# Kernel tuning notes

Hardware: AMD Instinct MI355X
Metric: run time of the kernel (lower is better)

Reference implementation:

```python
import jax, jax.numpy as jnp
import numpy as np

D_MODEL = 1024
N_HEAD = 16
D_K = D_MODEL // N_HEAD


def setup_inputs() -> dict:
    key = jax.random.key(0)
    ks = jax.random.split(key, 11)
    B, S, D = 2, 2048, D_MODEL
    scale = 1.0 / np.sqrt(D)
    inp = {
        "q": jax.random.normal(ks[0], (B, S, D), jnp.float32),
        "k": jax.random.normal(ks[1], (B, S, D), jnp.float32),
        "v": jax.random.normal(ks[2], (B, S, D), jnp.float32),
        "w_q": jax.random.normal(ks[3], (D, D), jnp.float32) * scale,
        "b_q": jnp.zeros((D,), jnp.float32),
        "w_k": jax.random.normal(ks[4], (D, D), jnp.float32) * scale,
        "b_k": jnp.zeros((D,), jnp.float32),
        "w_v": jax.random.normal(ks[5], (D, D), jnp.float32) * scale,
        "b_v": jnp.zeros((D,), jnp.float32),
        "w_o": jax.random.normal(ks[6], (D, D), jnp.float32) * scale,
        "b_o": jnp.zeros((D,), jnp.float32),
    }
    return inp


def _split_heads(x):
    # torch: chunk(n_head, dim=-1) then cat(dim=0) -> [H*B, S, d_k]
    B, S, D = x.shape
    x = x.reshape(B, S, N_HEAD, D_K)            # contiguous last-dim chunks
    return x.transpose(2, 0, 1, 3).reshape(N_HEAD * B, S, D_K)


def _merge_heads(x, B):
    # torch: chunk(n_head, dim=0) then cat(dim=-1) -> [B, S, D]
    HB, S, dk = x.shape
    x = x.reshape(N_HEAD, B, S, dk).transpose(1, 2, 0, 3)
    return x.reshape(B, S, N_HEAD * dk)


def reference(q, k, v, w_q, b_q, w_k, b_k, w_v, b_v, w_o, b_o):
    B = q.shape[0]
    qh = _split_heads(q @ w_q + b_q)            # [H*B, S, d_k]
    kh = _split_heads(k @ w_k + b_k)
    vh = _split_heads(v @ w_v + b_v)
    # scaled dot-product attention (naive, materializes scores)
    scores = jnp.einsum('bqd,bkd->bqk', qh, kh) / jnp.sqrt(jnp.float32(D_K))
    attn = jax.nn.softmax(scores, axis=-1)
    out = jnp.einsum('bqk,bkd->bqd', attn, vh)  # [H*B, S, d_k]
    out = _merge_heads(out, B)                  # [B, S, D]
    return out @ w_o + b_o
```

## Files before the change

kernel.cpp:

```cpp
#include <hip/hip_runtime.h>
#include <hip/hip_bf16.h>
#include <stdint.h>

#define DEVINL __device__ __forceinline__

typedef __attribute__((ext_vector_type(8))) short bf16x8;
typedef __attribute__((ext_vector_type(4))) short short4v;
typedef __attribute__((ext_vector_type(8))) unsigned short ushort8;
typedef __attribute__((ext_vector_type(4))) float f32x4;
typedef __attribute__((ext_vector_type(16))) float f32x16;

DEVINL unsigned short f2bf(float x) {
  union { float f; uint32_t u; } v; v.f = x;
  uint32_t u = v.u;
  u += 0x7fffu + ((u >> 16) & 1u);
  return (unsigned short)(u >> 16);
}

DEVINL uint32_t pack_bf16x2(float lo, float hi) {
  __hip_bfloat162 bb = __float22bfloat162_rn(make_float2(lo, hi));
  uint32_t r;
  __builtin_memcpy(&r, &bb, 4);
  return r;
}

DEVINL void gload_lds16(const void* g, void* l) {
  __builtin_amdgcn_global_load_lds((const __attribute__((address_space(1))) void*)g,
                                   (__attribute__((address_space(3))) void*)l, 16, 0, 0);
}

__global__ void cvt3_f32_bf16(const float* __restrict__ in0, unsigned short* __restrict__ out0,
                              const float* __restrict__ in1, unsigned short* __restrict__ out1,
                              const float* __restrict__ in2, unsigned short* __restrict__ out2,
                              int nper) {
  int nblk = gridDim.x / 3;
  int which = blockIdx.x / nblk;
  int i = ((blockIdx.x % nblk) * blockDim.x + threadIdx.x) * 8;
  if (i >= nper) return;
  const float* in = which == 0 ? in0 : which == 1 ? in1 : in2;
  unsigned short* out = which == 0 ? out0 : which == 1 ? out1 : out2;
  float4 a = *(const float4*)(in + i);
  float4 b = *(const float4*)(in + i + 4);
  ushort8 r;
  r[0] = f2bf(a.x); r[1] = f2bf(a.y); r[2] = f2bf(a.z); r[3] = f2bf(a.w);
  r[4] = f2bf(b.x); r[5] = f2bf(b.y); r[6] = f2bf(b.z); r[7] = f2bf(b.w);
  *(ushort8*)(out + i) = r;
}

__global__ __launch_bounds__(256) void transpose_w4(
    const float* __restrict__ w0, unsigned short* __restrict__ o0,
    const float* __restrict__ w1, unsigned short* __restrict__ o1,
    const float* __restrict__ w2, unsigned short* __restrict__ o2,
    const float* __restrict__ w3, unsigned short* __restrict__ o3) {
  __shared__ float tile[64][65];
  int z = blockIdx.z;
  const float* w = z == 0 ? w0 : z == 1 ? w1 : z == 2 ? w2 : w3;
  unsigned short* wt = z == 0 ? o0 : z == 1 ? o1 : z == 2 ? o2 : o3;
  int k0 = blockIdx.y * 64, n0 = blockIdx.x * 64;
  int t = threadIdx.x;
  for (int i = 0; i < 4; ++i) {
    int r = (t >> 4) + i * 16;
    int c = (t & 15) * 4;
    float4 v = *(const float4*)(w + (size_t)(k0 + r) * 1024 + n0 + c);
    tile[r][c] = v.x; tile[r][c + 1] = v.y; tile[r][c + 2] = v.z; tile[r][c + 3] = v.w;
  }
  __syncthreads();
  for (int i = 0; i < 4; ++i) {
    int rn = (t >> 4) + i * 16;
    int ck = (t & 15) * 4;
    short4v o;
    o[0] = (short)f2bf(tile[ck + 0][rn]);
    o[1] = (short)f2bf(tile[ck + 1][rn]);
    o[2] = (short)f2bf(tile[ck + 2][rn]);
    o[3] = (short)f2bf(tile[ck + 3][rn]);
    *(short4v*)(wt + (size_t)(n0 + rn) * 1024 + k0 + ck) = o;
  }
}

__global__ __launch_bounds__(256) void gemm_bt(
    const unsigned short* __restrict__ A,
    const unsigned short* __restrict__ Bt,
    const float* __restrict__ bias,
    void* __restrict__ out, float scale, int mode) {
  constexpr int K = 1024;
  __shared__ unsigned short Alds[2 * 128 * 32];
  __shared__ unsigned short Blds[2 * 64 * 32];
  int tile_m = blockIdx.x * 128;
  int tile_n = blockIdx.y * 64;
  int t = threadIdx.x, lane = t & 63, wid = t >> 6;
  int wm = wid >> 1, wn = wid & 1;
  int fr = lane & 15, fq = lane >> 4;
  f32x4 acc[4][2] = {};

  int ga0 = wid * 64 + lane, ga1 = ga0 + 256;
  int gb0 = wid * 64 + lane;
  int ra0 = ga0 >> 2, ca0 = ((ga0 & 3) ^ ((ra0 >> 1) & 3)) * 8;
  int ra1 = ga1 >> 2, ca1 = ((ga1 & 3) ^ ((ra1 >> 1) & 3)) * 8;
  int rb0 = gb0 >> 2, cb0 = ((gb0 & 3) ^ ((rb0 >> 1) & 3)) * 8;
  const unsigned short* Abase = A  + (size_t)tile_m * K;
  const unsigned short* Bbase = Bt + (size_t)tile_n * K;

  int aoff[4], boff[2];
#pragma unroll
  for (int i = 0; i < 4; ++i) {
    int r = wm * 64 + i * 16 + fr;
    aoff[i] = (r * 4 + (fq ^ ((r >> 1) & 3))) * 8;
  }
#pragma unroll
  for (int j = 0; j < 2; ++j) {
    int r = wn * 32 + j * 16 + fr;
    boff[j] = (r * 4 + (fq ^ ((r >> 1) & 3))) * 8;
  }

  auto stage = [&](int nb, int k0) {
    gload_lds16(Abase + (size_t)ra0 * K + k0 + ca0, Alds + nb * 4096 + ga0 * 8);
    gload_lds16(Abase + (size_t)ra1 * K + k0 + ca1, Alds + nb * 4096 + ga1 * 8);
    gload_lds16(Bbase + (size_t)rb0 * K + k0 + cb0, Blds + nb * 2048 + gb0 * 8);
  };
  auto compute = [&](int nb) {
    bf16x8 af[4], bfb[2];
#pragma unroll
    for (int i = 0; i < 4; ++i) af[i] = *(const bf16x8*)(Alds + nb * 4096 + aoff[i]);
#pragma unroll
    for (int j = 0; j < 2; ++j) bfb[j] = *(const bf16x8*)(Blds + nb * 2048 + boff[j]);
#pragma unroll
    for (int i = 0; i < 4; ++i)
#pragma unroll
      for (int j = 0; j < 2; ++j)
        acc[i][j] = __builtin_amdgcn_mfma_f32_16x16x32_bf16(af[i], bfb[j], acc[i][j], 0, 0, 0);
  };

  stage(0, 0);
  __syncthreads();
  for (int it = 0; it < 16; ++it) {
    int k1 = (2 * it + 1) * 32, k2 = (2 * it + 2) * 32;
    stage(1, k1);
    compute(0);
    __syncthreads();
    if (k2 < K) stage(0, k2);
    compute(1);
    __syncthreads();
  }

#pragma unroll
  for (int i = 0; i < 4; ++i) {
#pragma unroll
    for (int j = 0; j < 2; ++j) {
      int n = tile_n + wn * 32 + j * 16 + fr;
      float bv = bias[n];
      int m0 = tile_m + wm * 64 + i * 16 + fq * 4;
      if (mode == 0) {
        size_t base = (size_t)((n >> 6) * 2 + (m0 >> 11)) * (2048 * 64) + (n & 63);
#pragma unroll
        for (int r = 0; r < 4; ++r)
          ((unsigned short*)out)[base + (size_t)((m0 + r) & 2047) * 64] =
              f2bf((acc[i][j][r] + bv) * scale);
      } else if (mode == 2) {
        size_t base = (size_t)((n >> 6) * 2 + (m0 >> 11)) * (64 * 2048)
                    + (size_t)(n & 63) * 2048 + (m0 & 2047);
        short4v o;
#pragma unroll
        for (int r = 0; r < 4; ++r) o[r] = (short)f2bf(acc[i][j][r] + bv);
        *(short4v*)((unsigned short*)out + base) = o;
      } else {
#pragma unroll
        for (int r = 0; r < 4; ++r)
          ((float*)out)[(size_t)(m0 + r) * 1024 + n] = acc[i][j][r] + bv;
      }
    }
  }
}

__global__ __launch_bounds__(256) void attn_fwd(
    const unsigned short* __restrict__ Qh,
    const unsigned short* __restrict__ Kh,
    const unsigned short* __restrict__ Vtg,
    unsigned short* __restrict__ O) {
  constexpr int S = 2048, DK = 64;
  __shared__ unsigned short Klds[2 * 64 * 64];
  __shared__ unsigned short Vlds[2 * 64 * 64];
  __shared__ unsigned short Plds[4 * 32 * 72];

  int wg = blockIdx.x;
  int swz = (wg & 7) * 64 + (wg >> 3);
  int hb = swz >> 4;
  int qt = swz & 15;
  int t = threadIdx.x, lane = t & 63, wid = t >> 6;
  int lq = lane & 31, hi = lane >> 5;
  int q0 = qt * 128;

  const unsigned short* Qb = Qh  + (size_t)hb * S * DK;
  const unsigned short* Kb = Kh  + (size_t)hb * S * DK;
  const unsigned short* Vb = Vtg + (size_t)hb * DK * S;

  bf16x8 qf[4];
#pragma unroll
  for (int kk = 0; kk < 4; ++kk)
    qf[kk] = *(const bf16x8*)(Qb + (size_t)(q0 + wid * 32 + lq) * DK + kk * 16 + hi * 8);

  int g0 = wid * 128 + lane, g1 = g0 + 64;
  int sr0 = g0 >> 3, sc0 = ((g0 & 7) ^ (sr0 & 7)) * 8;
  int sr1 = g1 >> 3, sc1 = ((g1 & 7) ^ (sr1 & 7)) * 8;

  int koff[2][4], voff[2][4];
#pragma unroll
  for (int h2 = 0; h2 < 2; ++h2) {
    int row = 32 * h2 + lq;
#pragma unroll
    for (int kk = 0; kk < 4; ++kk)
      koff[h2][kk] = (row * 8 + ((2 * kk + hi) ^ (row & 7))) * 8;
  }
#pragma unroll
  for (int jt = 0; jt < 2; ++jt) {
    int row = 32 * jt + lq;
#pragma unroll
    for (int ks = 0; ks < 4; ++ks)
      voff[jt][ks] = (row * 8 + ((2 * ks + hi) ^ (row & 7))) * 8;
  }

  unsigned short* Pw = Plds + wid * (32 * 72) + lq * 72;

  auto stage = [&](int nb, int kt) {
    const unsigned short* Ksrc = Kb + (size_t)kt * 64 * DK;
    const unsigned short* Vsrc = Vb + (size_t)kt * 64;
    gload_lds16(Ksrc + sr0 * 64 + sc0, Klds + nb * 4096 + g0 * 8);
    gload_lds16(Ksrc + sr1 * 64 + sc1, Klds + nb * 4096 + g1 * 8);
    gload_lds16(Vsrc + (size_t)sr0 * S + sc0, Vlds + nb * 4096 + g0 * 8);
    gload_lds16(Vsrc + (size_t)sr1 * S + sc1, Vlds + nb * 4096 + g1 * 8);
  };

  float m = -INFINITY, l = 0.f;
  f32x16 oacc[2] = {};

  auto tilestep = [&](int nb) {
    const unsigned short* Kc = Klds + nb * 4096;
    const unsigned short* Vc = Vlds + nb * 4096;

    f32x16 sacc[2] = {};
#pragma unroll
    for (int kk = 0; kk < 4; ++kk) {
      bf16x8 k0 = *(const bf16x8*)(Kc + koff[0][kk]);
      sacc[0] = __builtin_amdgcn_mfma_f32_32x32x16_bf16(k0, qf[kk], sacc[0], 0, 0, 0);
      bf16x8 k1 = *(const bf16x8*)(Kc + koff[1][kk]);
      sacc[1] = __builtin_amdgcn_mfma_f32_32x32x16_bf16(k1, qf[kk], sacc[1], 0, 0, 0);
    }

    float pmax = fmaxf(sacc[0][0], sacc[0][1]);
#pragma unroll
    for (int r = 2; r < 16; r += 2) pmax = fmaxf(pmax, fmaxf(sacc[0][r], sacc[0][r + 1]));
#pragma unroll
    for (int r = 0; r < 16; r += 2) pmax = fmaxf(pmax, fmaxf(sacc[1][r], sacc[1][r + 1]));
    pmax = fmaxf(pmax, __shfl_xor(pmax, 32, 64));

    float mn = fmaxf(m, pmax);
    float cf = __expf(m - mn);
    m = mn;
    l *= cf;
#pragma unroll
    for (int jt = 0; jt < 2; ++jt)
#pragma unroll
      for (int r = 0; r < 16; ++r) oacc[jt][r] *= cf;

    float ps0 = 0.f, ps1 = 0.f;
#pragma unroll
    for (int r = 0; r < 16; ++r) {
      float p0 = __expf(sacc[0][r] - m);
      float p1 = __expf(sacc[1][r] - m);
      sacc[0][r] = p0; sacc[1][r] = p1;
      ps0 += p0; ps1 += p1;
    }
    float psum = ps0 + ps1;
    psum += __shfl_xor(psum, 32, 64);
    l += psum;

#pragma unroll
    for (int h2 = 0; h2 < 2; ++h2)
#pragma unroll
      for (int rp = 0; rp < 8; ++rp) {
        uint32_t w = pack_bf16x2(sacc[h2][2 * rp], sacc[h2][2 * rp + 1]);
        int key = 32 * h2 + 8 * (rp >> 1) + 4 * hi + 2 * (rp & 1);
        *(uint32_t*)(Pw + key) = w;
      }
    bf16x8 pfrag[4];
#pragma unroll
    for (int ks = 0; ks < 4; ++ks)
      pfrag[ks] = *(const bf16x8*)(Pw + 16 * ks + 8 * hi);

#pragma unroll
    for (int jt = 0; jt < 2; ++jt)
#pragma unroll
      for (int ks = 0; ks < 4; ++ks) {
        bf16x8 vf = *(const bf16x8*)(Vc + voff[jt][ks]);
        oacc[jt] = __builtin_amdgcn_mfma_f32_32x32x16_bf16(vf, pfrag[ks], oacc[jt], 0, 0, 0);
      }
  };

  stage(0, 0);
  __syncthreads();
  for (int it = 0; it < 16; ++it) {
    int t1 = 2 * it + 1, t2 = 2 * it + 2;
    stage(1, t1);
    tilestep(0);
    __syncthreads();
    if (t2 < 32) stage(0, t2);
    tilestep(1);
    __syncthreads();
  }

  int h = hb >> 1, b = hb & 1;
  int q = q0 + wid * 32 + lq;
  float linv = 1.0f / l;
  unsigned short* orow = O + (size_t)(b * 2048 + q) * 1024 + h * 64;
#pragma unroll
  for (int jt = 0; jt < 2; ++jt)
#pragma unroll
    for (int g = 0; g < 4; ++g) {
      short4v o;
#pragma unroll
      for (int r = 0; r < 4; ++r) o[r] = (short)f2bf(oacc[jt][4 * g + r] * linv);
      *(short4v*)(orow + jt * 32 + 8 * g + 4 * hi) = o;
    }
}

extern "C" void kernel_launch(void* const* d_in, const int* in_sizes, int n_in,
                              void* d_out, int out_size, void* d_ws, size_t ws_size,
                              hipStream_t stream) {
  const float* q   = (const float*)d_in[0];
  const float* k   = (const float*)d_in[1];
  const float* v   = (const float*)d_in[2];
  const float* w_q = (const float*)d_in[3];
  const float* b_q = (const float*)d_in[4];
  const float* w_k = (const float*)d_in[5];
  const float* b_k = (const float*)d_in[6];
  const float* w_v = (const float*)d_in[7];
  const float* b_v = (const float*)d_in[8];
  const float* w_o = (const float*)d_in[9];
  const float* b_o = (const float*)d_in[10];

  char* ws = (char*)d_ws;
  unsigned short* Xq  = (unsigned short*)(ws + 0);
  unsigned short* Xk  = (unsigned short*)(ws + 8388608);
  unsigned short* Xv  = (unsigned short*)(ws + 16777216);
  unsigned short* Wtq = (unsigned short*)(ws + 25165824);
  unsigned short* Wtk = (unsigned short*)(ws + 27262976);
  unsigned short* Wtv = (unsigned short*)(ws + 29360128);
  unsigned short* Wto = (unsigned short*)(ws + 31457280);
  unsigned short* Qh  = (unsigned short*)(ws + 33554432);
  unsigned short* Kh  = (unsigned short*)(ws + 41943040);
  unsigned short* Vt  = (unsigned short*)(ws + 50331648);
  unsigned short* Obuf = Xq;

  const int NACT = 4096 * 1024;
  cvt3_f32_bf16<<<3 * (NACT / 8 / 256), 256, 0, stream>>>(q, Xq, k, Xk, v, Xv, NACT);

  dim3 tg(16, 16, 4);
  transpose_w4<<<tg, 256, 0, stream>>>(w_q, Wtq, w_k, Wtk, w_v, Wtv, w_o, Wto);

  dim3 gg(32, 16);
  gemm_bt<<<gg, 256, 0, stream>>>(Xq, Wtq, b_q, Qh, 0.125f, 0);
  gemm_bt<<<gg, 256, 0, stream>>>(Xk, Wtk, b_k, Kh, 1.0f, 0);
  gemm_bt<<<gg, 256, 0, stream>>>(Xv, Wtv, b_v, Vt, 1.0f, 2);

  attn_fwd<<<512, 256, 0, stream>>>(Qh, Kh, Vt, Obuf);

  gemm_bt<<<gg, 256, 0, stream>>>(Obuf, Wto, b_o, d_out, 1.0f, 1);
}
```

Measured before the change: 169.3 us.

## Fuse QKV projections into one launch and use exp2 softmax with lazy rescale

Merges the three Q/K/V projection GEMMs into a single launch with a z-dimension that selects the operands, so the three run as one larger grid instead of three serial launches. It folds log2(e) into the Q scale so the softmax can use the hardware exp2 directly. It skips the running-max rescale of the output accumulator unless some lane's block max exceeds the stored max by more than 8, and splits the row-sum into four partial accumulators to shorten dependency chains. The lazy rescale lets exponentials reach up to 2^8 before renormalisation, which relies on fp32 headroom and bf16 packing of P staying accurate.

```diff
diff --git a/kernel.cpp b/kernel.cpp
--- a/kernel.cpp
+++ b/kernel.cpp
@@ -28,6 +28,8 @@
   __builtin_amdgcn_global_load_lds((const __attribute__((address_space(1))) void*)g,
                                    (__attribute__((address_space(3))) void*)l, 16, 0, 0);
 }
+
+#define E2(x) __builtin_amdgcn_exp2f(x)
 
 __global__ void cvt3_f32_bf16(const float* __restrict__ in0, unsigned short* __restrict__ out0,
                               const float* __restrict__ in1, unsigned short* __restrict__ out1,
@@ -77,16 +79,16 @@
   }
 }
 
-__global__ __launch_bounds__(256) void gemm_bt(
-    const unsigned short* __restrict__ A,
-    const unsigned short* __restrict__ Bt,
-    const float* __restrict__ bias,
-    void* __restrict__ out, float scale, int mode) {
+DEVINL void gemm_body(const unsigned short* __restrict__ A,
+                      const unsigned short* __restrict__ Bt,
+                      const float* __restrict__ bias,
+                      void* __restrict__ out, float scale, int mode,
+                      int bx, int by) {
   constexpr int K = 1024;
   __shared__ unsigned short Alds[2 * 128 * 32];
   __shared__ unsigned short Blds[2 * 64 * 32];
-  int tile_m = blockIdx.x * 128;
-  int tile_n = blockIdx.y * 64;
+  int tile_m = bx * 128;
+  int tile_n = by * 64;
   int t = threadIdx.x, lane = t & 63, wid = t >> 6;
   int wm = wid >> 1, wn = wid & 1;
   int fr = lane & 15, fq = lane >> 4;
@@ -171,6 +173,31 @@
   }
 }
 
+__global__ __launch_bounds__(256) void gemm_qkv(
+    const unsigned short* __restrict__ Xq, const unsigned short* __restrict__ Xk,
+    const unsigned short* __restrict__ Xv,
+    const unsigned short* __restrict__ Wtq, const unsigned short* __restrict__ Wtk,
+    const unsigned short* __restrict__ Wtv,
+    const float* __restrict__ bq, const float* __restrict__ bk,
+    const float* __restrict__ bv,
+    unsigned short* __restrict__ Qh, unsigned short* __restrict__ Kh,
+    unsigned short* __restrict__ Vt, float qscale) {
+  int z = blockIdx.z;
+  const unsigned short* A  = z == 0 ? Xq : z == 1 ? Xk : Xv;
+  const unsigned short* Bt = z == 0 ? Wtq : z == 1 ? Wtk : Wtv;
+  const float* bias        = z == 0 ? bq : z == 1 ? bk : bv;
+  void* out                = z == 0 ? (void*)Qh : z == 1 ? (void*)Kh : (void*)Vt;
+  float scale = z == 0 ? qscale : 1.0f;
+  int mode = z == 2 ? 2 : 0;
+  gemm_body(A, Bt, bias, out, scale, mode, blockIdx.x, blockIdx.y);
+}
+
+__global__ __launch_bounds__(256) void gemm_o(
+    const unsigned short* __restrict__ A, const unsigned short* __restrict__ Bt,
+    const float* __restrict__ bias, float* __restrict__ out) {
+  gemm_body(A, Bt, bias, out, 1.0f, 1, blockIdx.x, blockIdx.y);
+}
+
 __global__ __launch_bounds__(256) void attn_fwd(
     const unsigned short* __restrict__ Qh,
     const unsigned short* __restrict__ Kh,
@@ -252,24 +279,26 @@
     for (int r = 0; r < 16; r += 2) pmax = fmaxf(pmax, fmaxf(sacc[1][r], sacc[1][r + 1]));
     pmax = fmaxf(pmax, __shfl_xor(pmax, 32, 64));
 
-    float mn = fmaxf(m, pmax);
-    float cf = __expf(m - mn);
-    m = mn;
-    l *= cf;
-#pragma unroll
-    for (int jt = 0; jt < 2; ++jt)
-#pragma unroll
-      for (int r = 0; r < 16; ++r) oacc[jt][r] *= cf;
-
-    float ps0 = 0.f, ps1 = 0.f;
+    if (!__all(pmax <= m + 8.0f)) {
+      float mn = fmaxf(m, pmax);
+      float cf = E2(m - mn);
+      m = mn;
+      l *= cf;
+#pragma unroll
+      for (int jt = 0; jt < 2; ++jt)
+#pragma unroll
+        for (int r = 0; r < 16; ++r) oacc[jt][r] *= cf;
+    }
+
+    float ps[4] = {0.f, 0.f, 0.f, 0.f};
 #pragma unroll
     for (int r = 0; r < 16; ++r) {
-      float p0 = __expf(sacc[0][r] - m);
-      float p1 = __expf(sacc[1][r] - m);
+      float p0 = E2(sacc[0][r] - m);
+      float p1 = E2(sacc[1][r] - m);
       sacc[0][r] = p0; sacc[1][r] = p1;
-      ps0 += p0; ps1 += p1;
-    }
-    float psum = ps0 + ps1;
+      ps[r & 3] += p0 + p1;
+    }
+    float psum = (ps[0] + ps[1]) + (ps[2] + ps[3]);
     psum += __shfl_xor(psum, 32, 64);
     l += psum;
 
@@ -356,12 +385,13 @@
   dim3 tg(16, 16, 4);
   transpose_w4<<<tg, 256, 0, stream>>>(w_q, Wtq, w_k, Wtk, w_v, Wtv, w_o, Wto);
 
+  const float qscale = 0.125f * 1.44269504088896340736f;
+  dim3 gq(32, 16, 3);
+  gemm_qkv<<<gq, 256, 0, stream>>>(Xq, Xk, Xv, Wtq, Wtk, Wtv,
+                                   b_q, b_k, b_v, Qh, Kh, Vt, qscale);
+
+  attn_fwd<<<512, 256, 0, stream>>>(Qh, Kh, Vt, Obuf);
+
   dim3 gg(32, 16);
-  gemm_bt<<<gg, 256, 0, stream>>>(Xq, Wtq, b_q, Qh, 0.125f, 0);
-  gemm_bt<<<gg, 256, 0, stream>>>(Xk, Wtk, b_k, Kh, 1.0f, 0);
-  gemm_bt<<<gg, 256, 0, stream>>>(Xv, Wtv, b_v, Vt, 1.0f, 2);
-
-  attn_fwd<<<512, 256, 0, stream>>>(Qh, Kh, Vt, Obuf);
-
-  gemm_bt<<<gg, 256, 0, stream>>>(Obuf, Wto, b_o, d_out, 1.0f, 1);
-}
+  gemm_o<<<gg, 256, 0, stream>>>(Obuf, Wto, b_o, (float*)d_out);
+}
```

New measurement: 146.2 us. 1.16x faster.
